# Performance work log

Measured on AMD Instinct MI355X. Metric: run time of the kernel, lower is better.

## Reference

```python
import jax, jax.numpy as jnp
import numpy as np

BN_EPS = 1e-5


def setup_inputs() -> dict:
    key = jax.random.key(0)
    ks = jax.random.split(key, 12)
    B, N, G, D = 16, 8192, 64, 384
    C_IN = D + 64 + 3  # 451
    inp = {
        "features": jax.random.normal(ks[0], (B, G, D), jnp.float32),
        "centers": jax.random.normal(ks[1], (B, G, 3), jnp.float32),
        "pc": jax.random.normal(ks[2], (B, N, 3), jnp.float32),
        "category": jax.random.randint(ks[3], (B,), 0, 16, jnp.int64),
        "cat_embed": jax.random.normal(ks[4], (16, 64), jnp.float32) * 0.02,
        "w1": jax.random.normal(ks[5], (256, C_IN), jnp.float32) * (1.0 / np.sqrt(C_IN)),
        "b1": jnp.zeros((256,), jnp.float32),
        "g1": jnp.ones((256,), jnp.float32),
        "be1": jnp.zeros((256,), jnp.float32),
        "m1": jnp.zeros((256,), jnp.float32),
        "v1": jnp.ones((256,), jnp.float32),
        "w2": jax.random.normal(ks[6], (256, 256), jnp.float32) * (1.0 / 16.0),
        "b2": jnp.zeros((256,), jnp.float32),
        "g2": jnp.ones((256,), jnp.float32),
        "be2": jnp.zeros((256,), jnp.float32),
        "m2": jnp.zeros((256,), jnp.float32),
        "v2": jnp.ones((256,), jnp.float32),
        "w3": jax.random.normal(ks[7], (50, 256), jnp.float32) * (1.0 / 16.0),
        "b3": jnp.zeros((50,), jnp.float32),
    }
    return inp


def _bn(x, g, be, m, v):  # x: [B, N, C], inference-mode BatchNorm1d
    return (x - m) * (g * jax.lax.rsqrt(v + BN_EPS)) + be


def reference(features, centers, pc, category, cat_embed,
              w1, b1, g1, be1, m1, v1,
              w2, b2, g2, be2, m2, v2,
              w3, b3):
    B, N, _ = pc.shape
    # Euclidean cdist via norm expansion: [B, N, G]
    p2 = jnp.sum(pc * pc, axis=-1, keepdims=True)            # [B,N,1]
    c2 = jnp.sum(centers * centers, axis=-1)[:, None, :]     # [B,1,G]
    dot = jnp.einsum('bnd,bgd->bng', pc, centers)
    dist = jnp.sqrt(jnp.clip(p2 + c2 - 2.0 * dot, 1e-12))
    # top-3 smallest
    neg_d, knn_idx = jax.lax.top_k(-dist, 3)                 # [B,N,3]
    knn_dist = -neg_d
    w = 1.0 / (knn_dist + 1e-8)
    w = w / jnp.sum(w, axis=-1, keepdims=True)               # [B,N,3]
    # gather per-batch: features [B,G,D], knn_idx [B,N,3] -> [B,N,3,D]
    knn_features = jax.vmap(lambda f, i: f[i])(features, knn_idx)
    point_features = jnp.einsum('bnkd,bnk->bnd', knn_features, w)  # [B,N,D]
    cat_feat = jnp.broadcast_to(cat_embed[category][:, None, :], (B, N, 64))
    combined = jnp.concatenate([point_features, cat_feat, pc], axis=-1)  # [B,N,451]
    # Conv1d(k=1) == per-point dense layer; keep [B,N,C] layout
    h = jnp.einsum('bnc,oc->bno', combined, w1) + b1
    h = jax.nn.relu(_bn(h, g1, be1, m1, v1))
    h = jnp.einsum('bnc,oc->bno', h, w2) + b2
    h = jax.nn.relu(_bn(h, g2, be2, m2, v2))
    seg_logits = jnp.einsum('bnc,oc->bno', h, w3) + b3       # [B,N,50]
    return seg_logits
```

## Files before the change

### kernel.cpp

```cpp
#include <hip/hip_runtime.h>

#define TPB 256

typedef unsigned short u16;
typedef unsigned int u32;
typedef short short8 __attribute__((ext_vector_type(8)));
typedef float f32x4 __attribute__((ext_vector_type(4)));

#define KEEP(x) asm volatile("" :: "v"(x))

__device__ __forceinline__ u16 f2bf(float x) {
  union { float f; u32 u; } v;
  v.f = x;
  u32 r = v.u + 0x7FFFu + ((v.u >> 16) & 1u);
  return (u16)(r >> 16);
}

__device__ __forceinline__ float bf2f(u16 x) {
  union { u32 u; float f; } v;
  v.u = ((u32)x) << 16;
  return v.f;
}

__global__ void prep_kernel(const float* __restrict__ w1, const float* __restrict__ b1,
                            const float* __restrict__ g1, const float* __restrict__ be1,
                            const float* __restrict__ m1, const float* __restrict__ v1,
                            const float* __restrict__ w2, const float* __restrict__ b2,
                            const float* __restrict__ g2, const float* __restrict__ be2,
                            const float* __restrict__ m2, const float* __restrict__ v2,
                            const float* __restrict__ w3, const float* __restrict__ b3,
                            u16* __restrict__ w1b, u16* __restrict__ w2b, u16* __restrict__ w3b,
                            float* __restrict__ b1p, float* __restrict__ b2p, float* __restrict__ b3p)
{
  int i = blockIdx.x * TPB + threadIdx.x;
  if (i < 256 * 480) {
    int o = i / 480;
    int k = i - o * 480;
    float s = g1[o] * rsqrtf(v1[o] + 1e-5f);
    u16 r = 0;
    if (k < 451) r = f2bf(w1[o * 451 + k] * s);
    w1b[i] = r;
  }
  if (i < 256 * 256) {
    int o = i >> 8;
    float s = g2[o] * rsqrtf(v2[o] + 1e-5f);
    w2b[i] = f2bf(w2[i] * s);
  }
  if (i < 64 * 256) {
    int o = i >> 8;
    u16 r = 0;
    if (o < 50) r = f2bf(w3[i]);
    w3b[i] = r;
  }
  if (i < 256) {
    float s1 = g1[i] * rsqrtf(v1[i] + 1e-5f);
    b1p[i] = (b1[i] - m1[i]) * s1 + be1[i];
    float s2 = g2[i] * rsqrtf(v2[i] + 1e-5f);
    b2p[i] = (b2[i] - m2[i]) * s2 + be2[i];
  }
  if (i < 64) {
    b3p[i] = (i < 50) ? b3[i] : 0.f;
  }
}

__global__ __launch_bounds__(512, 2)
void gcalc_kernel(const float* __restrict__ features, const int* __restrict__ category,
                  const float* __restrict__ cat_embed, const u16* __restrict__ w1b,
                  const float* __restrict__ b1p,
                  u16* __restrict__ G, float* __restrict__ bias1)
{
  __shared__ u16 Fs[64 * 392];
  const int b    = blockIdx.x >> 1;
  const int och0 = (blockIdx.x & 1) * 128;
  const int tid  = threadIdx.x;
  const int lane = tid & 63;
  const int wv   = tid >> 6;
  const int lr   = lane & 15;
  const int lk   = (lane >> 4) * 8;
  const int r0   = (lane >> 4) * 4;
  const int catv = category[b];

  const f32x4* F4 = (const f32x4*)(features + b * 24576);
  #pragma unroll
  for (int it = 0; it < 12; ++it) {
    int idx = tid + 512 * it;
    int c = idx / 96;
    int d4 = idx - c * 96;
    f32x4 v = F4[c * 96 + d4];
    u32 lo = (u32)f2bf(v[0]) | ((u32)f2bf(v[1]) << 16);
    u32 hi = (u32)f2bf(v[2]) | ((u32)f2bf(v[3]) << 16);
    *(uint2*)&Fs[c * 392 + d4 * 4] = make_uint2(lo, hi);
  }

  if (tid < 128) {
    int o = och0 + tid;
    float acc = b1p[o];
    const u16* wr = w1b + o * 480 + 384;
    const float* ce = cat_embed + catv * 64;
    #pragma unroll 8
    for (int j = 0; j < 64; ++j) acc += bf2f(wr[j]) * ce[j];
    bias1[b * 256 + o] = acc;
    u16* Go = G + (b * 256 + o) * 96;
    Go[64] = wr[64]; Go[65] = wr[65]; Go[66] = wr[66];
    #pragma unroll
    for (int k = 67; k < 96; ++k) Go[k] = 0;
  }
  __syncthreads();

  const int ch = och0 + wv * 16 + lr;
  f32x4 acc[4];
  {
    f32x4 z = {0.f, 0.f, 0.f, 0.f};
    #pragma unroll
    for (int m = 0; m < 4; ++m) acc[m] = z;
  }
  #pragma unroll
  for (int ks = 0; ks < 12; ++ks) {
    short8 bv = *(const short8*)(w1b + ch * 480 + ks * 32 + lk);
    #pragma unroll
    for (int m = 0; m < 4; ++m) {
      short8 av = *(const short8*)(&Fs[(m * 16 + lr) * 392 + ks * 32 + lk]);
      acc[m] = __builtin_amdgcn_mfma_f32_16x16x32_bf16(av, bv, acc[m], 0, 0, 0);
    }
  }
  #pragma unroll
  for (int m = 0; m < 4; ++m)
    #pragma unroll
    for (int r = 0; r < 4; ++r)
      G[(b * 256 + ch) * 96 + m * 16 + r0 + r] = f2bf(acc[m][r]);
}

#define LDP 104
#define LDH 264

__global__ __launch_bounds__(512, 4)
void fused_kernel(const float* __restrict__ centers, const float* __restrict__ pc,
                  const u16* __restrict__ G, const float* __restrict__ bias1,
                  const u16* __restrict__ w2b, const u16* __restrict__ w3b,
                  const float* __restrict__ b2p, const float* __restrict__ b3p,
                  float* __restrict__ out)
{
  __shared__ u16 hbuf[128 * LDH];
  __shared__ float centl[192];
  __shared__ float pcl[384];

  const int bx   = blockIdx.x;
  const int b    = bx >> 6;
  const int n0   = (bx & 63) << 7;
  const int tid  = threadIdx.x;
  const int lane = tid & 63;
  const int wv   = tid >> 6;
  const int lr   = lane & 15;
  const int lk   = (lane >> 4) * 8;
  const int r0   = (lane >> 4) * 4;

  u16*   Pm   = hbuf;
  float* scrd = (float*)((char*)hbuf + 32768);
  int*   scri = (int*)((char*)hbuf + 40960);

  short8 bvG[3][2];
  #pragma unroll
  for (int ks = 0; ks < 3; ++ks)
    #pragma unroll
    for (int n = 0; n < 2; ++n)
      bvG[ks][n] = *(const short8*)(G + (b * 256 + wv * 32 + n * 16 + lr) * 96 + ks * 32 + lk);

  {
    u32* Pw = (u32*)Pm;
    #pragma unroll
    for (int i = 0; i < 13; ++i) Pw[tid + 512 * i] = 0;
  }
  if (tid < 192) centl[tid] = centers[b * 192 + tid];
  if (tid < 384) pcl[tid] = pc[(b * 8192 + n0) * 3 + tid];
  __syncthreads();

  {
    int p = tid >> 2, c = tid & 3;
    float px = pcl[p * 3 + 0], py = pcl[p * 3 + 1], pz = pcl[p * 3 + 2];
    float p2 = px * px + py * py + pz * pz;
    float bd0 = 3.4e38f, bd1 = 3.4e38f, bd2 = 3.4e38f;
    int bi0 = 0, bi1 = 0, bi2 = 0;
    int j0 = c * 16;
    for (int j = j0; j < j0 + 16; ++j) {
      float cx = centl[j * 3 + 0], cy = centl[j * 3 + 1], cz = centl[j * 3 + 2];
      float dotv = px * cx + py * cy + pz * cz;
      float c2 = cx * cx + cy * cy + cz * cz;
      float d2 = (p2 + c2) - 2.f * dotv;
      if (d2 < bd2) {
        if (d2 < bd1) {
          if (d2 < bd0) { bd2 = bd1; bi2 = bi1; bd1 = bd0; bi1 = bi0; bd0 = d2; bi0 = j; }
          else          { bd2 = bd1; bi2 = bi1; bd1 = d2; bi1 = j; }
        } else          { bd2 = d2; bi2 = j; }
      }
    }
    scrd[tid * 3 + 0] = bd0; scrd[tid * 3 + 1] = bd1; scrd[tid * 3 + 2] = bd2;
    scri[tid * 3 + 0] = bi0; scri[tid * 3 + 1] = bi1; scri[tid * 3 + 2] = bi2;
  }
  __syncthreads();

  if (tid < 128) {
    float bd0 = 3.4e38f, bd1 = 3.4e38f, bd2 = 3.4e38f;
    int bi0 = 0, bi1 = 0, bi2 = 0;
    #pragma unroll
    for (int c = 0; c < 4; ++c) {
      int t = tid * 4 + c;
      #pragma unroll
      for (int s = 0; s < 3; ++s) {
        float d2 = scrd[t * 3 + s];
        int   j  = scri[t * 3 + s];
        if (d2 < bd2) {
          if (d2 < bd1) {
            if (d2 < bd0) { bd2 = bd1; bi2 = bi1; bd1 = bd0; bi1 = bi0; bd0 = d2; bi0 = j; }
            else          { bd2 = bd1; bi2 = bi1; bd1 = d2; bi1 = j; }
          } else          { bd2 = d2; bi2 = j; }
        }
      }
    }
    float dd0 = sqrtf(fmaxf(bd0, 1e-12f));
    float dd1 = sqrtf(fmaxf(bd1, 1e-12f));
    float dd2 = sqrtf(fmaxf(bd2, 1e-12f));
    float u0 = 1.f / (dd0 + 1e-8f);
    float u1 = 1.f / (dd1 + 1e-8f);
    float u2 = 1.f / (dd2 + 1e-8f);
    float inv = 1.f / (u0 + u1 + u2);
    u16* Pr = Pm + tid * LDP;
    Pr[bi0] = f2bf(u0 * inv);
    Pr[bi1] = f2bf(u1 * inv);
    Pr[bi2] = f2bf(u2 * inv);
    Pr[64] = f2bf(pcl[tid * 3 + 0]);
    Pr[65] = f2bf(pcl[tid * 3 + 1]);
    Pr[66] = f2bf(pcl[tid * 3 + 2]);
  }
  KEEP(bvG[0][0]); KEEP(bvG[0][1]); KEEP(bvG[1][0]);
  KEEP(bvG[1][1]); KEEP(bvG[2][0]); KEEP(bvG[2][1]);
  __syncthreads();

  f32x4 acc[8][2];
  {
    f32x4 z = {0.f, 0.f, 0.f, 0.f};
    #pragma unroll
    for (int m = 0; m < 8; ++m) { acc[m][0] = z; acc[m][1] = z; }
  }
  #pragma unroll
  for (int ks = 0; ks < 3; ++ks) {
    short8 av[8];
    #pragma unroll
    for (int m = 0; m < 8; ++m)
      av[m] = *(const short8*)(&Pm[(m * 16 + lr) * LDP + ks * 32 + lk]);
    #pragma unroll
    for (int m = 0; m < 8; ++m)
      #pragma unroll
      for (int n = 0; n < 2; ++n)
        acc[m][n] = __builtin_amdgcn_mfma_f32_16x16x32_bf16(av[m], bvG[ks][n], acc[m][n], 0, 0, 0);
  }
  __syncthreads();

  #pragma unroll
  for (int n = 0; n < 2; ++n) {
    float bb = bias1[b * 256 + wv * 32 + n * 16 + lr];
    #pragma unroll
    for (int m = 0; m < 8; ++m)
      #pragma unroll
      for (int r = 0; r < 4; ++r) {
        float v = acc[m][n][r] + bb;
        v = v > 0.f ? v : 0.f;
        int row = m * 16 + r0 + r;
        int col = (wv * 32 + n * 16 + lr) ^ (((row >> 2) & 7) << 3);
        hbuf[row * LDH + col] = f2bf(v);
      }
  }
  __syncthreads();

  {
    f32x4 z = {0.f, 0.f, 0.f, 0.f};
    #pragma unroll
    for (int m = 0; m < 8; ++m) { acc[m][0] = z; acc[m][1] = z; }
  }
  #pragma unroll
  for (int ks = 0; ks < 8; ++ks) {
    short8 bv[2];
    #pragma unroll
    for (int n = 0; n < 2; ++n)
      bv[n] = *(const short8*)(w2b + (wv * 32 + n * 16 + lr) * 256 + ks * 32 + lk);
    short8 av[8];
    #pragma unroll
    for (int m = 0; m < 8; ++m) {
      int row = m * 16 + lr;
      int g = (ks * 4 + (lane >> 4)) ^ ((row >> 2) & 7);
      av[m] = *(const short8*)(&hbuf[row * LDH + g * 8]);
    }
    #pragma unroll
    for (int m = 0; m < 8; ++m)
      #pragma unroll
      for (int n = 0; n < 2; ++n)
        acc[m][n] = __builtin_amdgcn_mfma_f32_16x16x32_bf16(av[m], bv[n], acc[m][n], 0, 0, 0);
  }
  __syncthreads();

  #pragma unroll
  for (int n = 0; n < 2; ++n) {
    float bb = b2p[wv * 32 + n * 16 + lr];
    #pragma unroll
    for (int m = 0; m < 8; ++m)
      #pragma unroll
      for (int r = 0; r < 4; ++r) {
        float v = acc[m][n][r] + bb;
        v = v > 0.f ? v : 0.f;
        int row = m * 16 + r0 + r;
        int col = (wv * 32 + n * 16 + lr) ^ (((row >> 2) & 7) << 3);
        hbuf[row * LDH + col] = f2bf(v);
      }
  }

  const int wm = wv & 3;
  const int wn = wv >> 2;
  short8 w3f[8][2];
  #pragma unroll
  for (int ks = 0; ks < 8; ++ks)
    #pragma unroll
    for (int j = 0; j < 2; ++j)
      w3f[ks][j] = *(const short8*)(w3b + (wn * 32 + j * 16 + lr) * 256 + ks * 32 + lk);
  #pragma unroll
  for (int ks = 0; ks < 8; ++ks) { KEEP(w3f[ks][0]); KEEP(w3f[ks][1]); }
  __syncthreads();

  {
    f32x4 acc3[2][2];
    f32x4 z = {0.f, 0.f, 0.f, 0.f};
    acc3[0][0] = z; acc3[0][1] = z; acc3[1][0] = z; acc3[1][1] = z;
    #pragma unroll
    for (int ks = 0; ks < 8; ++ks) {
      #pragma unroll
      for (int mi = 0; mi < 2; ++mi) {
        int row = (wm * 2 + mi) * 16 + lr;
        int g = (ks * 4 + (lane >> 4)) ^ ((row >> 2) & 7);
        short8 av = *(const short8*)(&hbuf[row * LDH + g * 8]);
        #pragma unroll
        for (int j = 0; j < 2; ++j)
          acc3[mi][j] = __builtin_amdgcn_mfma_f32_16x16x32_bf16(av, w3f[ks][j], acc3[mi][j], 0, 0, 0);
      }
    }
    #pragma unroll
    for (int j = 0; j < 2; ++j) {
      int c = wn * 32 + j * 16 + lr;
      if (c < 50) {
        float b3v = b3p[c];
        #pragma unroll
        for (int mi = 0; mi < 2; ++mi)
          #pragma unroll
          for (int r = 0; r < 4; ++r) {
            int row = n0 + (wm * 2 + mi) * 16 + r0 + r;
            out[(b * 8192 + row) * 50 + c] = acc3[mi][j][r] + b3v;
          }
      }
    }
  }
}

extern "C" void kernel_launch(void* const* d_in, const int* in_sizes, int n_in,
                              void* d_out, int out_size, void* d_ws, size_t ws_size,
                              hipStream_t stream) {
  const float* features  = (const float*)d_in[0];
  const float* centers   = (const float*)d_in[1];
  const float* pc        = (const float*)d_in[2];
  const int*   category  = (const int*)d_in[3];
  const float* cat_embed = (const float*)d_in[4];
  const float* w1  = (const float*)d_in[5];
  const float* b1  = (const float*)d_in[6];
  const float* g1  = (const float*)d_in[7];
  const float* be1 = (const float*)d_in[8];
  const float* m1  = (const float*)d_in[9];
  const float* v1  = (const float*)d_in[10];
  const float* w2  = (const float*)d_in[11];
  const float* b2  = (const float*)d_in[12];
  const float* g2  = (const float*)d_in[13];
  const float* be2 = (const float*)d_in[14];
  const float* m2  = (const float*)d_in[15];
  const float* v2  = (const float*)d_in[16];
  const float* w3  = (const float*)d_in[17];
  const float* b3  = (const float*)d_in[18];
  float* out = (float*)d_out;

  char* ws = (char*)d_ws;
  u16*   w1b   = (u16*)(ws);
  u16*   w2b   = (u16*)(ws + 245760);
  u16*   w3b   = (u16*)(ws + 376832);
  float* b1p   = (float*)(ws + 409600);
  float* b2p   = (float*)(ws + 410624);
  float* b3p   = (float*)(ws + 411648);
  u16*   G     = (u16*)(ws + 412672);
  float* bias1 = (float*)(ws + 1199104);

  prep_kernel<<<480, TPB, 0, stream>>>(w1, b1, g1, be1, m1, v1,
                                       w2, b2, g2, be2, m2, v2,
                                       w3, b3, w1b, w2b, w3b, b1p, b2p, b3p);
  gcalc_kernel<<<32, 512, 0, stream>>>(features, category, cat_embed, w1b, b1p, G, bias1);

  fused_kernel<<<1024, 512, 0, stream>>>(centers, pc, G, bias1,
                                         w2b, w3b, b2p, b3p, out);
}
```

Before: 168.5 us.

## Merge weight prep into gcalc kernel and remap fused block order

Folds the prep kernel into the per-batch G computation, so W1 is read as fp32 and BN-scaled and converted on the fly. Extra blocks in the same launch handle the w2/w3/b2 conversion, and b3 is read directly. This removes one kernel launch and the serial prep-to-gcalc dependency, and gcalc now runs 64 blocks of 256 threads instead of 32 of 512. The fused kernel's block index is also swizzled so consecutive blocks cover different batches, which may change cache and XCD locality. In exchange, each gcalc block repeats the scale and convert work on its W1 rows.

```diff
diff --git a/kernel.cpp b/kernel.cpp
--- a/kernel.cpp
+++ b/kernel.cpp
@@ -1,6 +1,4 @@
 #include <hip/hip_runtime.h>
-
-#define TPB 256
 
 typedef unsigned short u16;
 typedef unsigned int u32;
@@ -8,6 +6,7 @@
 typedef float f32x4 __attribute__((ext_vector_type(4)));
 
 #define KEEP(x) asm volatile("" :: "v"(x))
+#define BN_EPS 1e-5f
 
 __device__ __forceinline__ u16 f2bf(float x) {
   union { float f; u32 u; } v;
@@ -16,118 +15,109 @@
   return (u16)(r >> 16);
 }
 
-__device__ __forceinline__ float bf2f(u16 x) {
-  union { u32 u; float f; } v;
-  v.u = ((u32)x) << 16;
-  return v.f;
-}
-
-__global__ void prep_kernel(const float* __restrict__ w1, const float* __restrict__ b1,
-                            const float* __restrict__ g1, const float* __restrict__ be1,
-                            const float* __restrict__ m1, const float* __restrict__ v1,
-                            const float* __restrict__ w2, const float* __restrict__ b2,
-                            const float* __restrict__ g2, const float* __restrict__ be2,
-                            const float* __restrict__ m2, const float* __restrict__ v2,
-                            const float* __restrict__ w3, const float* __restrict__ b3,
-                            u16* __restrict__ w1b, u16* __restrict__ w2b, u16* __restrict__ w3b,
-                            float* __restrict__ b1p, float* __restrict__ b2p, float* __restrict__ b3p)
-{
-  int i = blockIdx.x * TPB + threadIdx.x;
-  if (i < 256 * 480) {
-    int o = i / 480;
-    int k = i - o * 480;
-    float s = g1[o] * rsqrtf(v1[o] + 1e-5f);
-    u16 r = 0;
-    if (k < 451) r = f2bf(w1[o * 451 + k] * s);
-    w1b[i] = r;
-  }
-  if (i < 256 * 256) {
-    int o = i >> 8;
-    float s = g2[o] * rsqrtf(v2[o] + 1e-5f);
-    w2b[i] = f2bf(w2[i] * s);
-  }
-  if (i < 64 * 256) {
-    int o = i >> 8;
-    u16 r = 0;
-    if (o < 50) r = f2bf(w3[i]);
-    w3b[i] = r;
-  }
-  if (i < 256) {
-    float s1 = g1[i] * rsqrtf(v1[i] + 1e-5f);
-    b1p[i] = (b1[i] - m1[i]) * s1 + be1[i];
-    float s2 = g2[i] * rsqrtf(v2[i] + 1e-5f);
-    b2p[i] = (b2[i] - m2[i]) * s2 + be2[i];
-  }
-  if (i < 64) {
-    b3p[i] = (i < 50) ? b3[i] : 0.f;
-  }
-}
-
-__global__ __launch_bounds__(512, 2)
-void gcalc_kernel(const float* __restrict__ features, const int* __restrict__ category,
-                  const float* __restrict__ cat_embed, const u16* __restrict__ w1b,
-                  const float* __restrict__ b1p,
-                  u16* __restrict__ G, float* __restrict__ bias1)
+__global__ __launch_bounds__(256, 2)
+void gcalc_all(const float* __restrict__ features, const int* __restrict__ category,
+               const float* __restrict__ cat_embed,
+               const float* __restrict__ w1, const float* __restrict__ b1,
+               const float* __restrict__ g1, const float* __restrict__ be1,
+               const float* __restrict__ m1, const float* __restrict__ v1,
+               const float* __restrict__ w2, const float* __restrict__ g2,
+               const float* __restrict__ b2, const float* __restrict__ be2,
+               const float* __restrict__ m2, const float* __restrict__ v2,
+               const float* __restrict__ w3,
+               u16* __restrict__ G, float* __restrict__ bias1,
+               u16* __restrict__ w2b, u16* __restrict__ w3b, float* __restrict__ b2p)
 {
   __shared__ u16 Fs[64 * 392];
-  const int b    = blockIdx.x >> 1;
-  const int och0 = (blockIdx.x & 1) * 128;
-  const int tid  = threadIdx.x;
-  const int lane = tid & 63;
-  const int wv   = tid >> 6;
-  const int lr   = lane & 15;
-  const int lk   = (lane >> 4) * 8;
-  const int r0   = (lane >> 4) * 4;
-  const int catv = category[b];
-
-  const f32x4* F4 = (const f32x4*)(features + b * 24576);
-  #pragma unroll
-  for (int it = 0; it < 12; ++it) {
-    int idx = tid + 512 * it;
-    int c = idx / 96;
-    int d4 = idx - c * 96;
-    f32x4 v = F4[c * 96 + d4];
-    u32 lo = (u32)f2bf(v[0]) | ((u32)f2bf(v[1]) << 16);
-    u32 hi = (u32)f2bf(v[2]) | ((u32)f2bf(v[3]) << 16);
-    *(uint2*)&Fs[c * 392 + d4 * 4] = make_uint2(lo, hi);
-  }
-
-  if (tid < 128) {
-    int o = och0 + tid;
-    float acc = b1p[o];
-    const u16* wr = w1b + o * 480 + 384;
-    const float* ce = cat_embed + catv * 64;
-    #pragma unroll 8
-    for (int j = 0; j < 64; ++j) acc += bf2f(wr[j]) * ce[j];
-    bias1[b * 256 + o] = acc;
-    u16* Go = G + (b * 256 + o) * 96;
-    Go[64] = wr[64]; Go[65] = wr[65]; Go[66] = wr[66];
-    #pragma unroll
-    for (int k = 67; k < 96; ++k) Go[k] = 0;
-  }
-  __syncthreads();
-
-  const int ch = och0 + wv * 16 + lr;
-  f32x4 acc[4];
-  {
-    f32x4 z = {0.f, 0.f, 0.f, 0.f};
-    #pragma unroll
-    for (int m = 0; m < 4; ++m) acc[m] = z;
-  }
-  #pragma unroll
-  for (int ks = 0; ks < 12; ++ks) {
-    short8 bv = *(const short8*)(w1b + ch * 480 + ks * 32 + lk);
-    #pragma unroll
-    for (int m = 0; m < 4; ++m) {
-      short8 av = *(const short8*)(&Fs[(m * 16 + lr) * 392 + ks * 32 + lk]);
-      acc[m] = __builtin_amdgcn_mfma_f32_16x16x32_bf16(av, bv, acc[m], 0, 0, 0);
-    }
-  }
-  #pragma unroll
-  for (int m = 0; m < 4; ++m)
-    #pragma unroll
-    for (int r = 0; r < 4; ++r)
-      G[(b * 256 + ch) * 96 + m * 16 + r0 + r] = f2bf(acc[m][r]);
+  const int bid = blockIdx.x;
+  const int tid = threadIdx.x;
+
+  if (bid < 64) {
+    const int b    = bid >> 2;
+    const int och0 = (bid & 3) * 64;
+    const int lane = tid & 63;
+    const int wv   = tid >> 6;
+    const int lr   = lane & 15;
+    const int lk   = (lane >> 4) * 8;
+    const int r0   = (lane >> 4) * 4;
+
+    const f32x4* F4 = (const f32x4*)(features + b * 24576);
+    #pragma unroll
+    for (int it = 0; it < 24; ++it) {
+      int idx = tid + 256 * it;
+      int c = idx / 96;
+      int d4 = idx - c * 96;
+      f32x4 v = F4[c * 96 + d4];
+      u32 lo = (u32)f2bf(v[0]) | ((u32)f2bf(v[1]) << 16);
+      u32 hi = (u32)f2bf(v[2]) | ((u32)f2bf(v[3]) << 16);
+      *(uint2*)&Fs[c * 392 + d4 * 4] = make_uint2(lo, hi);
+    }
+
+    if (tid < 64) {
+      int o = och0 + tid;
+      float s1 = g1[o] * rsqrtf(v1[o] + BN_EPS);
+      float acc = (b1[o] - m1[o]) * s1 + be1[o];
+      const float* wr = w1 + o * 451 + 384;
+      const float* ce = cat_embed + category[b] * 64;
+      #pragma unroll 8
+      for (int j = 0; j < 64; ++j) acc += wr[j] * s1 * ce[j];
+      bias1[b * 256 + o] = acc;
+      u16* Go = G + (b * 256 + o) * 96;
+      Go[64] = f2bf(wr[64] * s1);
+      Go[65] = f2bf(wr[65] * s1);
+      Go[66] = f2bf(wr[66] * s1);
+      #pragma unroll
+      for (int k = 67; k < 96; ++k) Go[k] = 0;
+    }
+    __syncthreads();
+
+    const int ch = och0 + wv * 16 + lr;
+    const float s1 = g1[ch] * rsqrtf(v1[ch] + BN_EPS);
+    f32x4 acc[4];
+    {
+      f32x4 z = {0.f, 0.f, 0.f, 0.f};
+      #pragma unroll
+      for (int m = 0; m < 4; ++m) acc[m] = z;
+    }
+    #pragma unroll
+    for (int ks = 0; ks < 12; ++ks) {
+      const float* wr = w1 + ch * 451 + ks * 32 + lk;
+      short8 bv;
+      #pragma unroll
+      for (int e = 0; e < 8; ++e) bv[e] = (short)f2bf(wr[e] * s1);
+      #pragma unroll
+      for (int m = 0; m < 4; ++m) {
+        short8 av = *(const short8*)(&Fs[(m * 16 + lr) * 392 + ks * 32 + lk]);
+        acc[m] = __builtin_amdgcn_mfma_f32_16x16x32_bf16(av, bv, acc[m], 0, 0, 0);
+      }
+    }
+    #pragma unroll
+    for (int m = 0; m < 4; ++m)
+      #pragma unroll
+      for (int r = 0; r < 4; ++r)
+        G[(b * 256 + ch) * 96 + m * 16 + r0 + r] = f2bf(acc[m][r]);
+
+  } else if (bid < 80) {
+    int base = (bid - 64) * 4096;
+    #pragma unroll
+    for (int e = 0; e < 16; ++e) {
+      int i = base + e * 256 + tid;
+      int o = i >> 8;
+      float s2 = g2[o] * rsqrtf(v2[o] + BN_EPS);
+      w2b[i] = f2bf(w2[i] * s2);
+    }
+  } else {
+    #pragma unroll
+    for (int e = 0; e < 64; ++e) {
+      int i = e * 256 + tid;
+      int o = i >> 8;
+      w3b[i] = (o < 50) ? f2bf(w3[i]) : (u16)0;
+    }
+    {
+      float s2 = g2[tid] * rsqrtf(v2[tid] + BN_EPS);
+      b2p[tid] = (b2[tid] - m2[tid]) * s2 + be2[tid];
+    }
+  }
 }
 
 #define LDP 104
@@ -137,14 +127,14 @@
 void fused_kernel(const float* __restrict__ centers, const float* __restrict__ pc,
                   const u16* __restrict__ G, const float* __restrict__ bias1,
                   const u16* __restrict__ w2b, const u16* __restrict__ w3b,
-                  const float* __restrict__ b2p, const float* __restrict__ b3p,
+                  const float* __restrict__ b2p, const float* __restrict__ b3,
                   float* __restrict__ out)
 {
   __shared__ u16 hbuf[128 * LDH];
   __shared__ float centl[192];
   __shared__ float pcl[384];
 
-  const int bx   = blockIdx.x;
+  const int bx   = ((blockIdx.x & 7) << 7) | (blockIdx.x >> 3);
   const int b    = bx >> 6;
   const int n0   = (bx & 63) << 7;
   const int tid  = threadIdx.x;
@@ -344,7 +334,7 @@
     for (int j = 0; j < 2; ++j) {
       int c = wn * 32 + j * 16 + lr;
       if (c < 50) {
-        float b3v = b3p[c];
+        float b3v = b3[c];
         #pragma unroll
         for (int mi = 0; mi < 2; ++mi)
           #pragma unroll
@@ -382,20 +372,17 @@
   float* out = (float*)d_out;
 
   char* ws = (char*)d_ws;
-  u16*   w1b   = (u16*)(ws);
-  u16*   w2b   = (u16*)(ws + 245760);
-  u16*   w3b   = (u16*)(ws + 376832);
-  float* b1p   = (float*)(ws + 409600);
-  float* b2p   = (float*)(ws + 410624);
-  float* b3p   = (float*)(ws + 411648);
-  u16*   G     = (u16*)(ws + 412672);
-  float* bias1 = (float*)(ws + 1199104);
-
-  prep_kernel<<<480, TPB, 0, stream>>>(w1, b1, g1, be1, m1, v1,
-                                       w2, b2, g2, be2, m2, v2,
-                                       w3, b3, w1b, w2b, w3b, b1p, b2p, b3p);
-  gcalc_kernel<<<32, 512, 0, stream>>>(features, category, cat_embed, w1b, b1p, G, bias1);
+  u16*   w2b   = (u16*)(ws);
+  u16*   w3b   = (u16*)(ws + 131072);
+  float* b2p   = (float*)(ws + 163840);
+  u16*   G     = (u16*)(ws + 164864);
+  float* bias1 = (float*)(ws + 951296);
+
+  gcalc_all<<<81, 256, 0, stream>>>(features, category, cat_embed,
+                                    w1, b1, g1, be1, m1, v1,
+                                    w2, g2, b2, be2, m2, v2, w3,
+                                    G, bias1, w2b, w3b, b2p);
 
   fused_kernel<<<1024, 512, 0, stream>>>(centers, pc, G, bias1,
-                                         w2b, w3b, b2p, b3p, out);
+                                         w2b, w3b, b2p, b3, out);
 }
```

Result: no change. 169.4 us (+0.5%).
